# Kernel tuning notes

Hardware: AMD Instinct MI355X
Metric: run time of the kernel (lower is better)

Reference implementation:

```python
import jax, jax.numpy as jnp
import numpy as np
import math

EMBED_DIM = 1024
NUM_HEADS = 16
HEAD_DIM = EMBED_DIM // NUM_HEADS
SEGMENT_LENGTHS = [2048, 4096]
DILATION_RATES = [1, 2]
B, N = 1, 8192
IS_CAUSAL = True


def setup_inputs() -> dict:
    key = jax.random.key(0)
    ks = jax.random.split(key, 12)
    def w(k):
        return (jax.random.normal(k, (EMBED_DIM, EMBED_DIM), dtype=jnp.float32) * 0.02)
    inp = {
        'query': jax.random.normal(ks[0], (B, N, EMBED_DIM), dtype=jnp.float32),
        'key':   jax.random.normal(ks[1], (B, N, EMBED_DIM), dtype=jnp.float32),
        'value': jax.random.normal(ks[2], (B, N, EMBED_DIM), dtype=jnp.float32),
        'Wq': w(ks[3]), 'bq': jnp.zeros((EMBED_DIM,), jnp.float32),
        'Wk': w(ks[4]), 'bk': jnp.zeros((EMBED_DIM,), jnp.float32),
        'Wv': w(ks[5]), 'bv': jnp.zeros((EMBED_DIM,), jnp.float32),
        'Wo': w(ks[6]), 'bo': jnp.zeros((EMBED_DIM,), jnp.float32),
    }
    return inp


def _dilated_group_attention(q, k, v, seg_len, dilation, offset, causal):
    # q,k,v: [B, N, Hg, D] -> dilated block attention within segments
    b, n, hg, d = q.shape
    nseg = n // seg_len
    m = seg_len // dilation  # dilated subsequence length per segment
    idx = offset + dilation * jnp.arange(m)  # positions inside a segment
    def gather(x):
        return x.reshape(b, nseg, seg_len, hg, d)[:, :, idx]  # [B,nseg,m,Hg,D]
    qs, ks_, vs = gather(q), gather(k), gather(v)
    scale = 1.0 / math.sqrt(d)
    # [B,nseg,Hg,m,m]
    scores = jnp.einsum('bnihd,bnjhd->bnhij', qs, ks_) * scale
    if causal:
        mask = jnp.tril(jnp.ones((m, m), dtype=bool))
        scores = jnp.where(mask, scores, jnp.finfo(scores.dtype).min)
    attn = jax.nn.softmax(scores, axis=-1)
    out = jnp.einsum('bnhij,bnjhd->bnihd', attn, vs)  # [B,nseg,m,Hg,D]
    # scatter dilated outputs back to full segment positions (others zero)
    full = jnp.zeros((b, nseg, seg_len, hg, d), dtype=out.dtype)
    full = full.at[:, :, idx].set(out)
    return full.reshape(b, n, hg, d)


def reference(query, key, value, Wq, bq, Wk, bk, Wv, bv, Wo, bo):
    b, n, e = query.shape
    q = query @ Wq.T + bq
    k = key @ Wk.T + bk
    v = value @ Wv.T + bv
    q = q.reshape(b, n, NUM_HEADS, HEAD_DIM)
    k = k.reshape(b, n, NUM_HEADS, HEAD_DIM)
    v = v.reshape(b, n, NUM_HEADS, HEAD_DIM)
    num_groups = len(SEGMENT_LENGTHS)
    hpg = NUM_HEADS // num_groups  # heads per (segment, dilation) group
    outs = []
    for g in range(num_groups):
        s, r = SEGMENT_LENGTHS[g], DILATION_RATES[g]
        off = g % r
        hsl = slice(g * hpg, (g + 1) * hpg)
        outs.append(_dilated_group_attention(q[:, :, hsl], k[:, :, hsl], v[:, :, hsl],
                                             s, r, off, IS_CAUSAL))
    attn_out = jnp.concatenate(outs, axis=2).reshape(b, n, e)
    return attn_out @ Wo.T + bo
```

## Files before the change

kernel.cpp:

```cpp
#include <hip/hip_runtime.h>
#include <hip/hip_bf16.h>

typedef __attribute__((ext_vector_type(8))) __bf16 bf16x8;
typedef __attribute__((ext_vector_type(8))) unsigned short us8;
typedef __attribute__((ext_vector_type(4))) float f32x4;
typedef __attribute__((ext_vector_type(16))) float f32x16;
typedef __attribute__((ext_vector_type(2))) unsigned int uint2v;

#define N_TOK 8192
#define EMB 1024
#define SC2F 0.18033688011112042f

static __device__ __forceinline__ unsigned short f2bf(float f) {
  union { __bf16 b; unsigned short u; } c;
  c.b = (__bf16)f;
  return c.u;
}

static __device__ __forceinline__ f32x4 mfma16(bf16x8 a, bf16x8 b, f32x4 c) {
  return __builtin_amdgcn_mfma_f32_16x16x32_bf16(a, b, c, 0, 0, 0);
}
static __device__ __forceinline__ f32x16 mfma32(bf16x8 a, bf16x8 b, f32x16 c) {
  return __builtin_amdgcn_mfma_f32_32x32x16_bf16(a, b, c, 0, 0, 0);
}
static __device__ __forceinline__ unsigned int cvtpk(float lo, float hi) {
  unsigned int r;
  asm("v_cvt_pk_bf16_f32 %0, %1, %2" : "=v"(r) : "v"(lo), "v"(hi));
  return r;
}
static __device__ __forceinline__ void gload16(const unsigned short* g, unsigned short* l) {
  __builtin_amdgcn_global_load_lds(
      (const __attribute__((address_space(1))) unsigned int*)g,
      (__attribute__((address_space(3))) unsigned int*)l, 16, 0, 0);
}

__global__ __launch_bounds__(256) void convall(
    const float* __restrict__ X0, const float* __restrict__ X1, const float* __restrict__ X2,
    const float* __restrict__ W0, const float* __restrict__ W1,
    const float* __restrict__ W2, const float* __restrict__ W3,
    unsigned short* __restrict__ Dq, unsigned short* __restrict__ Dk,
    unsigned short* __restrict__ Dv, unsigned short* __restrict__ Wb)
{
  const int bid = blockIdx.x;
  const float* src;
  unsigned short* dst;
  long base;
  if (bid < 6144) {
    const int t = bid >> 11;
    const int b = bid & 2047;
    src = (t == 0) ? X0 : (t == 1) ? X1 : X2;
    dst = (t == 0) ? Dq : (t == 1) ? Dk : Dv;
    base = ((long)b * 256 + threadIdx.x) * 16;
  } else {
    const int r = bid - 6144;
    const int t = r >> 8;
    const int b = r & 255;
    src = (t == 0) ? W0 : (t == 1) ? W1 : (t == 2) ? W2 : W3;
    dst = Wb + (size_t)t * EMB * EMB;
    base = ((long)b * 256 + threadIdx.x) * 16;
  }
  float4 f0 = *(const float4*)(src + base);
  float4 f1 = *(const float4*)(src + base + 4);
  float4 f2 = *(const float4*)(src + base + 8);
  float4 f3 = *(const float4*)(src + base + 12);
  us8 p0, p1;
  p0[0]=f2bf(f0.x); p0[1]=f2bf(f0.y); p0[2]=f2bf(f0.z); p0[3]=f2bf(f0.w);
  p0[4]=f2bf(f1.x); p0[5]=f2bf(f1.y); p0[6]=f2bf(f1.z); p0[7]=f2bf(f1.w);
  p1[0]=f2bf(f2.x); p1[1]=f2bf(f2.y); p1[2]=f2bf(f2.z); p1[3]=f2bf(f2.w);
  p1[4]=f2bf(f3.x); p1[5]=f2bf(f3.y); p1[6]=f2bf(f3.z); p1[7]=f2bf(f3.w);
  *(us8*)(dst + base)     = p0;
  *(us8*)(dst + base + 8) = p1;
}

__global__ __launch_bounds__(256) void zerog1(unsigned short* __restrict__ AO)
{
  const int idx = blockIdx.x * 256 + threadIdx.x;
  const int row = idx >> 6;
  const int c8  = (idx & 63) * 8;
  const us8 zz = {0,0,0,0,0,0,0,0};
  *(us8*)(AO + (long)(row * 2) * EMB + 512 + c8) = zz;
}

__global__ __launch_bounds__(256) void qkv_gemm7(
    const unsigned short* __restrict__ Xq, const unsigned short* __restrict__ Xk,
    const unsigned short* __restrict__ Xv, const unsigned short* __restrict__ Wb,
    const float* __restrict__ bq, const float* __restrict__ bk, const float* __restrict__ bv,
    unsigned short* __restrict__ O0, unsigned short* __restrict__ O1, unsigned short* __restrict__ O2)
{
  __shared__ __align__(16) unsigned short As[128 * 32];
  __shared__ __align__(16) unsigned short Bs[128 * 32];

  const int z = blockIdx.z;
  const unsigned short* X = (z == 0) ? Xq : (z == 1) ? Xk : Xv;
  const unsigned short* W = Wb + (size_t)z * EMB * EMB;
  const float* bias = (z == 0) ? bq : (z == 1) ? bk : bv;

  const int lin  = blockIdx.x;
  const int work = (lin & 7) * 64 + (lin >> 3);
  const long brow = (long)(work >> 3) * 128;
  const long bcol = (long)(work & 7) * 128;

  const int tid  = threadIdx.x;
  const int lane = tid & 63;
  const int w    = tid >> 6;
  const int wrb  = (w >> 1) * 64;
  const int wcb  = (w & 1) * 64;
  const int r16  = lane & 15;
  const int kq   = (lane >> 4) * 8;
  const int rq   = (lane >> 4) * 4;

  const int srow = lane >> 2;
  const int scol = (lane & 3) * 8;
  const unsigned short* Ag0 = X + (brow + w*32      + srow) * (long)EMB + scol;
  const unsigned short* Ag1 = X + (brow + w*32 + 16 + srow) * (long)EMB + scol;
  const unsigned short* Bg0 = W + (bcol + w*32      + srow) * (long)EMB + scol;
  const unsigned short* Bg1 = W + (bcol + w*32 + 16 + srow) * (long)EMB + scol;
  unsigned short* Al0 = As + w * 1024;
  unsigned short* Al1 = As + w * 1024 + 512;
  unsigned short* Bl0 = Bs + w * 1024;
  unsigned short* Bl1 = Bs + w * 1024 + 512;

  const f32x4 zz = {0.f, 0.f, 0.f, 0.f};
  f32x4 acc[4][4];
#pragma unroll
  for (int i = 0; i < 4; ++i)
#pragma unroll
    for (int j = 0; j < 4; ++j) acc[i][j] = zz;

  for (int k0 = 0; k0 < EMB; k0 += 32) {
    __syncthreads();
    gload16(Ag0 + k0, Al0);
    gload16(Ag1 + k0, Al1);
    gload16(Bg0 + k0, Bl0);
    gload16(Bg1 + k0, Bl1);
    __syncthreads();

    bf16x8 av[4], bv_[4];
#pragma unroll
    for (int mi = 0; mi < 4; ++mi) av[mi]  = *(const bf16x8*)&As[(wrb + mi*16 + r16)*32 + kq];
#pragma unroll
    for (int ni = 0; ni < 4; ++ni) bv_[ni] = *(const bf16x8*)&Bs[(wcb + ni*16 + r16)*32 + kq];
    if (z == 2) {
#pragma unroll
      for (int mi = 0; mi < 4; ++mi)
#pragma unroll
        for (int ni = 0; ni < 4; ++ni)
          acc[mi][ni] = mfma16(bv_[ni], av[mi], acc[mi][ni]);
    } else {
#pragma unroll
      for (int mi = 0; mi < 4; ++mi)
#pragma unroll
        for (int ni = 0; ni < 4; ++ni)
          acc[mi][ni] = mfma16(av[mi], bv_[ni], acc[mi][ni]);
    }
  }

  if (z == 2) {
#pragma unroll
    for (int ni = 0; ni < 4; ++ni)
#pragma unroll
      for (int jr = 0; jr < 4; ++jr) {
        const long c = bcol + wcb + ni*16 + rq + jr;
        const float bval = bias[c];
#pragma unroll
        for (int mi = 0; mi < 4; ++mi) {
          long rt = brow + wrb + mi*16 + r16;
          if (c >= 512) {
            const long seg = rt >> 12;
            const long pp = rt & 4095;
            rt = (seg << 12) + ((pp & 1) ? (pp >> 1) : 2048 + (pp >> 1));
          }
          O2[c * (long)N_TOK + rt] = f2bf(acc[mi][ni][jr] + bval);
        }
      }
  } else {
    unsigned short* O = (z == 0) ? O0 : O1;
#pragma unroll
    for (int ni = 0; ni < 4; ++ni) {
      const long col = bcol + wcb + ni*16 + r16;
      const float bval = bias[col];
#pragma unroll
      for (int mi = 0; mi < 4; ++mi)
#pragma unroll
        for (int jr = 0; jr < 4; ++jr) {
          const long row = brow + wrb + mi*16 + rq + jr;
          float v = acc[mi][ni][jr] + bval;
          if (z == 0) v *= SC2F;
          O[row * (long)EMB + col] = f2bf(v);
        }
    }
  }
}

__global__ __launch_bounds__(128) void attn_dilated10(
    const unsigned short* __restrict__ Qp, const unsigned short* __restrict__ Kp,
    const unsigned short* __restrict__ Vt, unsigned short* __restrict__ AO)
{
  __shared__ __align__(16) unsigned short Ks[2][64][76];
  __shared__ __align__(16) unsigned short Vs[2][64][76];

  const int z   = blockIdx.z;
  const int g1  = (z >= 4);
  const int dil = g1 ? 2 : 1;
  const int off = g1 ? 1 : 0;
  const long segb = g1 ? (long)(z - 4) * 4096 : (long)z * 2048;
  const int h   = (g1 ? 8 : 0) + blockIdx.y;
  const int h64 = h * 64;

  const int bx   = (int)blockIdx.x;
  const int tid  = threadIdx.x;
  const int lane = tid & 63;
  const int w    = tid >> 6;
  const int q5   = lane & 31;
  const int hh   = lane >> 5;

  const int srow = tid >> 1;
  const int sc   = (tid & 1) * 32;

#pragma unroll
  for (int ph = 0; ph < 2; ++ph) {
    const int hf = ph ? bx : 31 - bx;
    const int qq = hf*64 + w*32 + q5;
    const long qrow = segb + off + (long)dil * qq;

    bf16x8 qf[4];
    {
      const unsigned short* qsrc = Qp + qrow * EMB + h64 + 8*hh;
#pragma unroll
      for (int s = 0; s < 4; ++s) qf[s] = *(const bf16x8*)(qsrc + 16*s);
    }

    float l_run = 0.f;
    f32x16 o0, o1;
#pragma unroll
    for (int r = 0; r < 16; ++r) { o0[r] = 0.f; o1[r] = 0.f; }

    us8 kr0, kr1, kr2, kr3, vr0, vr1, vr2, vr3;
    {
      const long gk = segb + off + (long)dil * srow;
      const unsigned short* ksrc = Kp + gk*EMB + h64 + sc;
      kr0 = *(const us8*)ksrc;        kr1 = *(const us8*)(ksrc + 8);
      kr2 = *(const us8*)(ksrc + 16); kr3 = *(const us8*)(ksrc + 24);
      const unsigned short* vsrc = Vt + (long)(h64 + srow)*N_TOK + segb + sc;
      vr0 = *(const us8*)vsrc;        vr1 = *(const us8*)(vsrc + 8);
      vr2 = *(const us8*)(vsrc + 16); vr3 = *(const us8*)(vsrc + 24);
      *(us8*)&Ks[0][srow][sc]    = kr0; *(us8*)&Ks[0][srow][sc+8]  = kr1;
      *(us8*)&Ks[0][srow][sc+16] = kr2; *(us8*)&Ks[0][srow][sc+24] = kr3;
      *(us8*)&Vs[0][srow][sc]    = vr0; *(us8*)&Vs[0][srow][sc+8]  = vr1;
      *(us8*)&Vs[0][srow][sc+16] = vr2; *(us8*)&Vs[0][srow][sc+24] = vr3;
    }
    __syncthreads();
    int cur = 0;

    for (int j = 0; j <= hf; ++j) {
      if (j < hf) {
        const long gk = segb + off + (long)dil * ((j+1)*64 + srow);
        const unsigned short* ksrc = Kp + gk*EMB + h64 + sc;
        kr0 = *(const us8*)ksrc;        kr1 = *(const us8*)(ksrc + 8);
        kr2 = *(const us8*)(ksrc + 16); kr3 = *(const us8*)(ksrc + 24);
        const unsigned short* vsrc = Vt + (long)(h64 + srow)*N_TOK + segb + (j+1)*64 + sc;
        vr0 = *(const us8*)vsrc;        vr1 = *(const us8*)(vsrc + 8);
        vr2 = *(const us8*)(vsrc + 16); vr3 = *(const us8*)(vsrc + 24);
      }

      f32x16 sa0, sa1;
#pragma unroll
      for (int r = 0; r < 16; ++r) { sa0[r] = 0.f; sa1[r] = 0.f; }
      __builtin_amdgcn_s_setprio(1);
#pragma unroll
      for (int s = 0; s < 4; ++s) {
        bf16x8 ka = *(const bf16x8*)&Ks[cur][q5][16*s + 8*hh];
        sa0 = mfma32(ka, qf[s], sa0);
      }
#pragma unroll
      for (int s = 0; s < 4; ++s) {
        bf16x8 kb = *(const bf16x8*)&Ks[cur][32 + q5][16*s + 8*hh];
        sa1 = mfma32(kb, qf[s], sa1);
      }
      __builtin_amdgcn_s_setprio(0);

      const bool diag   = (j == hf);
      const bool do_kb1 = (j < hf) || (w == 1);

      float sv[32];
#pragma unroll
      for (int r = 0; r < 16; ++r) {
        const int kof = (r&3) + 8*(r>>2);
        float v = sa0[r];
        if (diag && (j*64 + kof + 4*hh > qq)) v = -1e30f;
        sv[r] = v;
      }
      if (do_kb1) {
#pragma unroll
        for (int r = 0; r < 16; ++r) {
          const int kof = (r&3) + 8*(r>>2);
          float v = sa1[r];
          if (diag && (j*64 + 32 + kof + 4*hh > qq)) v = -1e30f;
          sv[16+r] = v;
        }
      }

      float ps0 = 0.f, ps1 = 0.f, ps2 = 0.f, ps3 = 0.f;
#pragma unroll
      for (int i = 0; i < 16; i += 4) {
        float e0 = exp2f(sv[i]);   sv[i]   = e0; ps0 += e0;
        float e1 = exp2f(sv[i+1]); sv[i+1] = e1; ps1 += e1;
        float e2 = exp2f(sv[i+2]); sv[i+2] = e2; ps2 += e2;
        float e3 = exp2f(sv[i+3]); sv[i+3] = e3; ps3 += e3;
      }
      if (do_kb1) {
#pragma unroll
        for (int i = 16; i < 32; i += 4) {
          float e0 = exp2f(sv[i]);   sv[i]   = e0; ps0 += e0;
          float e1 = exp2f(sv[i+1]); sv[i+1] = e1; ps1 += e1;
          float e2 = exp2f(sv[i+2]); sv[i+2] = e2; ps2 += e2;
          float e3 = exp2f(sv[i+3]); sv[i+3] = e3; ps3 += e3;
        }
      }
      float psum = (ps0 + ps1) + (ps2 + ps3);
      {
        union { float f; unsigned int u; } pc; pc.f = psum;
        uint2v ps = __builtin_amdgcn_permlane32_swap(pc.u, pc.u, false, false);
        union { unsigned int u; float f; } a0, a1;
        a0.u = ps[0]; a1.u = ps[1];
        psum = a0.f + a1.f;
      }
      l_run += psum;

#pragma unroll
      for (int ks = 0; ks < 4; ++ks) {
        if (ks >= 2 && !do_kb1) continue;
        const unsigned int pk0 = cvtpk(sv[8*ks+0], sv[8*ks+1]);
        const unsigned int pk1 = cvtpk(sv[8*ks+2], sv[8*ks+3]);
        const unsigned int pk2 = cvtpk(sv[8*ks+4], sv[8*ks+5]);
        const unsigned int pk3 = cvtpk(sv[8*ks+6], sv[8*ks+7]);
        uint2v s02 = __builtin_amdgcn_permlane32_swap(pk0, pk2, false, false);
        uint2v s13 = __builtin_amdgcn_permlane32_swap(pk1, pk3, false, false);
        union { unsigned int wd[4]; bf16x8 v; } pu;
        pu.wd[0] = s02[0];
        pu.wd[1] = s13[0];
        pu.wd[2] = s02[1];
        pu.wd[3] = s13[1];
        __builtin_amdgcn_s_setprio(1);
        bf16x8 va = *(const bf16x8*)&Vs[cur][q5][16*ks + 8*hh];
        o0 = mfma32(va, pu.v, o0);
        bf16x8 vb = *(const bf16x8*)&Vs[cur][32 + q5][16*ks + 8*hh];
        o1 = mfma32(vb, pu.v, o1);
        __builtin_amdgcn_s_setprio(0);
      }

      if (j < hf) {
        *(us8*)&Ks[cur^1][srow][sc]    = kr0; *(us8*)&Ks[cur^1][srow][sc+8]  = kr1;
        *(us8*)&Ks[cur^1][srow][sc+16] = kr2; *(us8*)&Ks[cur^1][srow][sc+24] = kr3;
        *(us8*)&Vs[cur^1][srow][sc]    = vr0; *(us8*)&Vs[cur^1][srow][sc+8]  = vr1;
        *(us8*)&Vs[cur^1][srow][sc+16] = vr2; *(us8*)&Vs[cur^1][srow][sc+24] = vr3;
      }
      __syncthreads();
      cur ^= 1;
    }

    {
      const float inv = 1.f / l_run;
      unsigned short* dst = AO + qrow * EMB + h64;
#pragma unroll
      for (int r = 0; r < 16; ++r) {
        const int d = (r&3) + 8*(r>>2) + 4*hh;
        dst[d]      = f2bf(o0[r] * inv);
        dst[32 + d] = f2bf(o1[r] * inv);
      }
    }
  }
}

__global__ __launch_bounds__(256) void gemm_out4(
    const unsigned short* __restrict__ A, const unsigned short* __restrict__ Wb,
    const float* __restrict__ bias, float* __restrict__ outp)
{
  __shared__ __align__(16) unsigned short As[128 * 32];
  __shared__ __align__(16) unsigned short Bs[128 * 32];

  const int lin  = blockIdx.x;
  const int work = (lin & 7) * 64 + (lin >> 3);
  const long brow = (long)(work >> 3) * 128;
  const long bcol = (long)(work & 7) * 128;

  const int tid  = threadIdx.x;
  const int lane = tid & 63;
  const int w    = tid >> 6;
  const int wrb  = (w >> 1) * 64;
  const int wcb  = (w & 1) * 64;
  const int r16  = lane & 15;
  const int kq   = (lane >> 4) * 8;
  const int rq   = (lane >> 4) * 4;

  const int srow = lane >> 2;
  const int scol = (lane & 3) * 8;
  const unsigned short* Ag0 = A  + (brow + w*32      + srow) * (long)EMB + scol;
  const unsigned short* Ag1 = A  + (brow + w*32 + 16 + srow) * (long)EMB + scol;
  const unsigned short* Bg0 = Wb + (bcol + w*32      + srow) * (long)EMB + scol;
  const unsigned short* Bg1 = Wb + (bcol + w*32 + 16 + srow) * (long)EMB + scol;
  unsigned short* Al0 = As + w * 1024;
  unsigned short* Al1 = As + w * 1024 + 512;
  unsigned short* Bl0 = Bs + w * 1024;
  unsigned short* Bl1 = Bs + w * 1024 + 512;

  const f32x4 zz = {0.f, 0.f, 0.f, 0.f};
  f32x4 acc[4][4];
#pragma unroll
  for (int i = 0; i < 4; ++i)
#pragma unroll
    for (int j = 0; j < 4; ++j) acc[i][j] = zz;

  for (int k0 = 0; k0 < EMB; k0 += 32) {
    __syncthreads();
    gload16(Ag0 + k0, Al0);
    gload16(Ag1 + k0, Al1);
    gload16(Bg0 + k0, Bl0);
    gload16(Bg1 + k0, Bl1);
    __syncthreads();

    bf16x8 av[4], bv_[4];
#pragma unroll
    for (int mi = 0; mi < 4; ++mi) av[mi]  = *(const bf16x8*)&As[(wrb + mi*16 + r16)*32 + kq];
#pragma unroll
    for (int ni = 0; ni < 4; ++ni) bv_[ni] = *(const bf16x8*)&Bs[(wcb + ni*16 + r16)*32 + kq];
#pragma unroll
    for (int mi = 0; mi < 4; ++mi)
#pragma unroll
      for (int ni = 0; ni < 4; ++ni)
        acc[mi][ni] = mfma16(av[mi], bv_[ni], acc[mi][ni]);
  }

#pragma unroll
  for (int ni = 0; ni < 4; ++ni) {
    const long col = bcol + wcb + ni*16 + r16;
    const float bval = bias[col];
#pragma unroll
    for (int mi = 0; mi < 4; ++mi)
#pragma unroll
      for (int jr = 0; jr < 4; ++jr) {
        const long row = brow + wrb + mi*16 + rq + jr;
        outp[row * (long)EMB + col] = acc[mi][ni][jr] + bval;
      }
  }
}

extern "C" void kernel_launch(void* const* d_in, const int* in_sizes, int n_in,
                              void* d_out, int out_size, void* d_ws, size_t ws_size,
                              hipStream_t stream) {
  const float* query = (const float*)d_in[0];
  const float* key_  = (const float*)d_in[1];
  const float* value = (const float*)d_in[2];
  const float* Wq = (const float*)d_in[3];
  const float* bq = (const float*)d_in[4];
  const float* Wk = (const float*)d_in[5];
  const float* bk = (const float*)d_in[6];
  const float* Wv = (const float*)d_in[7];
  const float* bv = (const float*)d_in[8];
  const float* Wo = (const float*)d_in[9];
  const float* bo = (const float*)d_in[10];

  unsigned short* Qp  = (unsigned short*)d_ws;
  unsigned short* Kp  = Qp + (size_t)N_TOK * EMB;
  unsigned short* Vt  = Kp + (size_t)N_TOK * EMB;
  unsigned short* Wb  = Vt + (size_t)N_TOK * EMB;
  unsigned short* S   = Wb + (size_t)4 * EMB * EMB;
  unsigned short* Xbq = (unsigned short*)d_out;
  unsigned short* Xbk = Xbq + (size_t)N_TOK * EMB;
  unsigned short* Xbv = S;
  unsigned short* AO  = S;
  unsigned short* Wob = Wb + (size_t)3 * EMB * EMB;

  dim3 blk(256);

  hipLaunchKernelGGL(convall, dim3(7168), blk, 0, stream,
                     query, key_, value, Wq, Wk, Wv, Wo, Xbq, Xbk, Xbv, Wb);

  hipLaunchKernelGGL(qkv_gemm7, dim3(512, 1, 3), blk, 0, stream,
                     Xbq, Xbk, Xbv, Wb, bq, bk, bv, Qp, Kp, Vt);

  hipLaunchKernelGGL(zerog1, dim3(1024), blk, 0, stream, AO);

  hipLaunchKernelGGL(attn_dilated10, dim3(16, 8, 6), dim3(128), 0, stream, Qp, Kp, Vt, AO);

  hipLaunchKernelGGL(gemm_out4, dim3(512), blk, 0, stream, AO, Wob, bo, (float*)d_out);
}
```

Before: 206.7 us.

## Process both causal query tiles concurrently in one 256-thread attention block

The attention kernel previously ran two phases in sequence per block, one for a long query tile (31-bx) and one for a short tile (bx), each streaming its own K/V tiles. Now the block has four waves: two handle the long tile and two the short tile, and they share a single K/V stream through shared memory, so the short tile's K/V loads are reused from the long tile's pass. Each thread now loads half as much K/V per tile. The short-tile waves idle once they pass their diagonal but still have to join the barriers, and more threads per block may reduce the number of resident blocks per CU.

```diff
diff --git a/kernel.cpp b/kernel.cpp
--- a/kernel.cpp
+++ b/kernel.cpp
@@ -192,7 +192,7 @@
   }
 }
 
-__global__ __launch_bounds__(128) void attn_dilated10(
+__global__ __launch_bounds__(256) void attn_dilated11(
     const unsigned short* __restrict__ Qp, const unsigned short* __restrict__ Kp,
     const unsigned short* __restrict__ Vt, unsigned short* __restrict__ AO)
 {
@@ -214,55 +214,49 @@
   const int q5   = lane & 31;
   const int hh   = lane >> 5;
 
-  const int srow = tid >> 1;
-  const int sc   = (tid & 1) * 32;
-
-#pragma unroll
-  for (int ph = 0; ph < 2; ++ph) {
-    const int hf = ph ? bx : 31 - bx;
-    const int qq = hf*64 + w*32 + q5;
-    const long qrow = segb + off + (long)dil * qq;
-
-    bf16x8 qf[4];
-    {
-      const unsigned short* qsrc = Qp + qrow * EMB + h64 + 8*hh;
-#pragma unroll
-      for (int s = 0; s < 4; ++s) qf[s] = *(const bf16x8*)(qsrc + 16*s);
-    }
-
-    float l_run = 0.f;
-    f32x16 o0, o1;
-#pragma unroll
-    for (int r = 0; r < 16; ++r) { o0[r] = 0.f; o1[r] = 0.f; }
-
-    us8 kr0, kr1, kr2, kr3, vr0, vr1, vr2, vr3;
-    {
-      const long gk = segb + off + (long)dil * srow;
+  const int hfL = 31 - bx;
+  const int hfw = (w < 2) ? hfL : bx;
+  const int qq  = hfw*64 + (w & 1)*32 + q5;
+  const long qrow = segb + off + (long)dil * qq;
+
+  bf16x8 qf[4];
+  {
+    const unsigned short* qsrc = Qp + qrow * EMB + h64 + 8*hh;
+#pragma unroll
+    for (int s = 0; s < 4; ++s) qf[s] = *(const bf16x8*)(qsrc + 16*s);
+  }
+
+  float l_run = 0.f;
+  f32x16 o0, o1;
+#pragma unroll
+  for (int r = 0; r < 16; ++r) { o0[r] = 0.f; o1[r] = 0.f; }
+
+  const int srow = tid >> 2;
+  const int sc   = (tid & 3) * 16;
+
+  us8 kr0, kr1, vr0, vr1;
+  {
+    const long gk = segb + off + (long)dil * srow;
+    const unsigned short* ksrc = Kp + gk*EMB + h64 + sc;
+    kr0 = *(const us8*)ksrc; kr1 = *(const us8*)(ksrc + 8);
+    const unsigned short* vsrc = Vt + (long)(h64 + srow)*N_TOK + segb + sc;
+    vr0 = *(const us8*)vsrc; vr1 = *(const us8*)(vsrc + 8);
+    *(us8*)&Ks[0][srow][sc]   = kr0; *(us8*)&Ks[0][srow][sc+8] = kr1;
+    *(us8*)&Vs[0][srow][sc]   = vr0; *(us8*)&Vs[0][srow][sc+8] = vr1;
+  }
+  __syncthreads();
+  int cur = 0;
+
+  for (int j = 0; j <= hfL; ++j) {
+    if (j < hfL) {
+      const long gk = segb + off + (long)dil * ((j+1)*64 + srow);
       const unsigned short* ksrc = Kp + gk*EMB + h64 + sc;
-      kr0 = *(const us8*)ksrc;        kr1 = *(const us8*)(ksrc + 8);
-      kr2 = *(const us8*)(ksrc + 16); kr3 = *(const us8*)(ksrc + 24);
-      const unsigned short* vsrc = Vt + (long)(h64 + srow)*N_TOK + segb + sc;
-      vr0 = *(const us8*)vsrc;        vr1 = *(const us8*)(vsrc + 8);
-      vr2 = *(const us8*)(vsrc + 16); vr3 = *(const us8*)(vsrc + 24);
-      *(us8*)&Ks[0][srow][sc]    = kr0; *(us8*)&Ks[0][srow][sc+8]  = kr1;
-      *(us8*)&Ks[0][srow][sc+16] = kr2; *(us8*)&Ks[0][srow][sc+24] = kr3;
-      *(us8*)&Vs[0][srow][sc]    = vr0; *(us8*)&Vs[0][srow][sc+8]  = vr1;
-      *(us8*)&Vs[0][srow][sc+16] = vr2; *(us8*)&Vs[0][srow][sc+24] = vr3;
-    }
-    __syncthreads();
-    int cur = 0;
-
-    for (int j = 0; j <= hf; ++j) {
-      if (j < hf) {
-        const long gk = segb + off + (long)dil * ((j+1)*64 + srow);
-        const unsigned short* ksrc = Kp + gk*EMB + h64 + sc;
-        kr0 = *(const us8*)ksrc;        kr1 = *(const us8*)(ksrc + 8);
-        kr2 = *(const us8*)(ksrc + 16); kr3 = *(const us8*)(ksrc + 24);
-        const unsigned short* vsrc = Vt + (long)(h64 + srow)*N_TOK + segb + (j+1)*64 + sc;
-        vr0 = *(const us8*)vsrc;        vr1 = *(const us8*)(vsrc + 8);
-        vr2 = *(const us8*)(vsrc + 16); vr3 = *(const us8*)(vsrc + 24);
-      }
-
+      kr0 = *(const us8*)ksrc; kr1 = *(const us8*)(ksrc + 8);
+      const unsigned short* vsrc = Vt + (long)(h64 + srow)*N_TOK + segb + (j+1)*64 + sc;
+      vr0 = *(const us8*)vsrc; vr1 = *(const us8*)(vsrc + 8);
+    }
+
+    if (j <= hfw) {
       f32x16 sa0, sa1;
 #pragma unroll
       for (int r = 0; r < 16; ++r) { sa0[r] = 0.f; sa1[r] = 0.f; }
@@ -279,8 +273,8 @@
       }
       __builtin_amdgcn_s_setprio(0);
 
-      const bool diag   = (j == hf);
-      const bool do_kb1 = (j < hf) || (w == 1);
+      const bool diag   = (j == hfw);
+      const bool do_kb1 = (j < hfw) || ((w & 1) == 1);
 
       float sv[32];
 #pragma unroll
@@ -348,26 +342,24 @@
         o1 = mfma32(vb, pu.v, o1);
         __builtin_amdgcn_s_setprio(0);
       }
-
-      if (j < hf) {
-        *(us8*)&Ks[cur^1][srow][sc]    = kr0; *(us8*)&Ks[cur^1][srow][sc+8]  = kr1;
-        *(us8*)&Ks[cur^1][srow][sc+16] = kr2; *(us8*)&Ks[cur^1][srow][sc+24] = kr3;
-        *(us8*)&Vs[cur^1][srow][sc]    = vr0; *(us8*)&Vs[cur^1][srow][sc+8]  = vr1;
-        *(us8*)&Vs[cur^1][srow][sc+16] = vr2; *(us8*)&Vs[cur^1][srow][sc+24] = vr3;
-      }
-      __syncthreads();
-      cur ^= 1;
-    }
-
-    {
-      const float inv = 1.f / l_run;
-      unsigned short* dst = AO + qrow * EMB + h64;
-#pragma unroll
-      for (int r = 0; r < 16; ++r) {
-        const int d = (r&3) + 8*(r>>2) + 4*hh;
-        dst[d]      = f2bf(o0[r] * inv);
-        dst[32 + d] = f2bf(o1[r] * inv);
-      }
+    }
+
+    if (j < hfL) {
+      *(us8*)&Ks[cur^1][srow][sc]   = kr0; *(us8*)&Ks[cur^1][srow][sc+8] = kr1;
+      *(us8*)&Vs[cur^1][srow][sc]   = vr0; *(us8*)&Vs[cur^1][srow][sc+8] = vr1;
+    }
+    __syncthreads();
+    cur ^= 1;
+  }
+
+  {
+    const float inv = 1.f / l_run;
+    unsigned short* dst = AO + qrow * EMB + h64;
+#pragma unroll
+    for (int r = 0; r < 16; ++r) {
+      const int d = (r&3) + 8*(r>>2) + 4*hh;
+      dst[d]      = f2bf(o0[r] * inv);
+      dst[32 + d] = f2bf(o1[r] * inv);
     }
   }
 }
@@ -481,7 +473,7 @@
 
   hipLaunchKernelGGL(zerog1, dim3(1024), blk, 0, stream, AO);
 
-  hipLaunchKernelGGL(attn_dilated10, dim3(16, 8, 6), dim3(128), 0, stream, Qp, Kp, Vt, AO);
+  hipLaunchKernelGGL(attn_dilated11, dim3(16, 8, 6), blk, 0, stream, Qp, Kp, Vt, AO);
 
   hipLaunchKernelGGL(gemm_out4, dim3(512), blk, 0, stream, AO, Wob, bo, (float*)d_out);
 }
```

After: 253.3 us. 1.23x slower.
